# Optimization experiments

Measured on AMD Instinct MI355X. Metric: run time of the kernel, lower is better.

Reference implementation:

```python
import jax, jax.numpy as jnp
import numpy as np

EPS = 1e-5


def _two_qubit_block(xa, xb, pa, pb, ga, gb):
    """Analytic 2-qubit state-vector sim (real amplitudes, Ry/CNOT only).
    Circuit: Ry(xa)q0, Ry(xb)q1, Ry(pa)q0, Ry(pb)q1, CNOT(0,1), Ry(ga)q0, Ry(gb)q1.
    Returns (<Z0>, <Z1>) batched over xa/xb shape."""
    ha = 0.5 * (xa + pa)  # consecutive Ry angles add
    hb = 0.5 * (xb + pb)
    ca, sa = jnp.cos(ha), jnp.sin(ha)
    cb, sb = jnp.cos(hb), jnp.sin(hb)
    # product state amplitudes psi[i,j]
    p00, p01, p10, p11 = ca * cb, ca * sb, sa * cb, sa * sb
    # CNOT(control=0, target=1): swap |10> <-> |11>
    p10, p11 = p11, p10
    # Ry(ga) on qubit 0
    cg, sg = jnp.cos(0.5 * ga), jnp.sin(0.5 * ga)
    q00 = cg * p00 - sg * p10
    q10 = sg * p00 + cg * p10
    q01 = cg * p01 - sg * p11
    q11 = sg * p01 + cg * p11
    # Ry(gb) on qubit 1
    ch, sh = jnp.cos(0.5 * gb), jnp.sin(0.5 * gb)
    r00 = ch * q00 - sh * q01
    r01 = sh * q00 + ch * q01
    r10 = ch * q10 - sh * q11
    r11 = sh * q10 + ch * q11
    z0 = r00 ** 2 + r01 ** 2 - r10 ** 2 - r11 ** 2
    z1 = r00 ** 2 - r01 ** 2 + r10 ** 2 - r11 ** 2
    return z0, z1


def _forward(x, qparams, in_proj_w, in_proj_b, out_proj_w, out_proj_b,
             ln_w, ln_b, lin_w, lin_b):
    B = x.shape[0]
    xi = x.reshape(B, 28, 28)
    # extract 2x2 patches in order [x[r,c], x[r,c+1], x[r+1,c], x[r+1,c+1]]
    patches = xi.reshape(B, 14, 2, 14, 2).transpose(0, 1, 3, 2, 4).reshape(B, 196, 4)
    # vectorized quantum kernel: qubits (0,1) and (2,3) are independent 2-qubit blocks
    z0, z1 = _two_qubit_block(patches[..., 0], patches[..., 1],
                              qparams[0], qparams[1], qparams[4], qparams[5])
    z2, z3 = _two_qubit_block(patches[..., 2], patches[..., 3],
                              qparams[2], qparams[3], qparams[6], qparams[7])
    seq = jnp.stack([z0, z1, z2, z3], axis=-1)  # (B, 196, 4)

    # MultiheadAttention: embed_dim=4, heads=2, head_dim=2 (eval mode, no dropout)
    E, H, D, L = 4, 2, 2, 196
    qkv = seq @ in_proj_w.T + in_proj_b  # (B, L, 12)
    q, k, v = jnp.split(qkv, 3, axis=-1)
    q = q.reshape(B, L, H, D)
    k = k.reshape(B, L, H, D)
    v = v.reshape(B, L, H, D)
    scores = jnp.einsum('blhd,bmhd->bhlm', q, k) / jnp.sqrt(jnp.asarray(D, q.dtype))
    attn = jax.nn.softmax(scores, axis=-1)
    o = jnp.einsum('bhlm,bmhd->blhd', attn, v).reshape(B, L, E)
    o = o @ out_proj_w.T + out_proj_b  # (B, L, 4)

    # LayerNorm over the channel dim (size 4)
    mu = o.mean(axis=-1, keepdims=True)
    var = o.var(axis=-1, keepdims=True)
    o = (o - mu) / jnp.sqrt(var + EPS) * ln_w + ln_b

    # permute to (B, 4, 196) then flatten to match linear's 4*14*14 layout
    flat = o.transpose(0, 2, 1).reshape(B, 4 * 196)
    logits = flat @ lin_w.T + lin_b
    return jax.nn.log_softmax(logits, axis=-1)


def setup_inputs() -> dict:
    key = jax.random.key(0)
    ks = jax.random.split(key, 8)
    B, E, L = 2048, 4, 196
    x = jax.random.uniform(ks[0], (B, 1, 28, 28), dtype=jnp.float32)
    qparams = jax.random.normal(ks[1], (8,), dtype=jnp.float32)
    in_proj_w = jax.random.normal(ks[2], (3 * E, E), dtype=jnp.float32) * (1.0 / np.sqrt(E))
    in_proj_b = jnp.zeros((3 * E,), dtype=jnp.float32)
    out_proj_w = jax.random.normal(ks[3], (E, E), dtype=jnp.float32) * (1.0 / np.sqrt(E))
    out_proj_b = jnp.zeros((E,), dtype=jnp.float32)
    ln_w = jnp.ones((E,), dtype=jnp.float32)
    ln_b = jnp.zeros((E,), dtype=jnp.float32)
    lin_w = jax.random.normal(ks[4], (10, E * L), dtype=jnp.float32) * (1.0 / np.sqrt(E * L))
    lin_b = jnp.zeros((10,), dtype=jnp.float32)
    return {"x": x, "qparams": qparams, "in_proj_w": in_proj_w, "in_proj_b": in_proj_b,
            "out_proj_w": out_proj_w, "out_proj_b": out_proj_b,
            "ln_w": ln_w, "ln_b": ln_b, "lin_w": lin_w, "lin_b": lin_b}


def reference(x, qparams, in_proj_w, in_proj_b, out_proj_w, out_proj_b,
              ln_w, ln_b, lin_w, lin_b):
    return _forward(x, qparams, in_proj_w, in_proj_b, out_proj_w, out_proj_b,
                    ln_w, ln_b, lin_w, lin_b)
```

## Files before the change

### kernel.cpp

```cpp
#include <hip/hip_runtime.h>
#include <hip/hip_bf16.h>

#define NTHREADS 256
#define EPSF 1e-5f
#define QSCALE 1.0201606003163899f

typedef float v2f __attribute__((ext_vector_type(2)));
typedef float v4f __attribute__((ext_vector_type(4)));

#if __has_builtin(__builtin_amdgcn_exp2f)
#define EXP2F(x) __builtin_amdgcn_exp2f(x)
#else
extern "C" __device__ float __ocml_native_exp2_f32(float);
#define EXP2F(x) __ocml_native_exp2_f32(x)
#endif

__device__ __forceinline__ void two_qubit(float xa, float xb, float pa, float pb,
                                          float cg, float sg, float ch, float sh,
                                          float& z0, float& z1) {
    const float ha = 0.5f * (xa + pa);
    const float hb = 0.5f * (xb + pb);
    float sa, ca, sb, cb;
    __sincosf(ha, &sa, &ca);
    __sincosf(hb, &sb, &cb);
    const float p00 = ca * cb, p01 = ca * sb;
    const float p10 = sa * sb, p11 = sa * cb;
    const float q00 = cg * p00 - sg * p10;
    const float q10 = sg * p00 + cg * p10;
    const float q01 = cg * p01 - sg * p11;
    const float q11 = sg * p01 + cg * p11;
    const float r00 = ch * q00 - sh * q01;
    const float r01 = sh * q00 + ch * q01;
    const float r10 = ch * q10 - sh * q11;
    const float r11 = sh * q10 + ch * q11;
    const float a = r00 * r00, b = r01 * r01, c = r10 * r10, d = r11 * r11;
    z0 = a + b - c - d;
    z1 = a - b + c - d;
}

__global__ __launch_bounds__(NTHREADS, 8)
void quanv_fused(const float* __restrict__ x,
                 const float* __restrict__ qparams,
                 const float* __restrict__ in_w,
                 const float* __restrict__ in_b,
                 const float* __restrict__ out_w,
                 const float* __restrict__ out_b,
                 const float* __restrict__ lnw,
                 const float* __restrict__ lnb,
                 const float* __restrict__ lin_w,
                 const float* __restrict__ lin_b,
                 float* __restrict__ out)
{
    __shared__ __align__(16) float uni[2352];
    __shared__ __align__(16) float2 qs[2][196];
    __shared__ v4f kT[2][98];
    __shared__ v4f vT[2][98];
    __shared__ float w_in[48], b_in[12], w_out[16], b_out[4];
    __shared__ float s_lnw[4], s_lnb[4], s_linb[10];
    __shared__ float qc[8];
    __shared__ float qp[4];
    __shared__ float wsum[4][10];
    __shared__ float logits_s[10];
    __shared__ float lse_s;

    float* psum = uni;
    float* pa0  = uni + 784;
    float* pa1  = uni + 1568;
    float* flat = (float*)qs;

    const int tid = threadIdx.x;
    const int bid = blockIdx.x;

    const float4* xb4 = (const float4*)(x + (size_t)bid * 784);
    if (tid < 196) ((float4*)uni)[tid] = xb4[tid];
    if (tid < 48) w_in[tid] = in_w[tid];
    {
        int t = tid - 64;  if (t >= 0 && t < 12) b_in[t] = in_b[t];
        t = tid - 80;      if (t >= 0 && t < 16) w_out[t] = out_w[t];
        t = tid - 96;      if (t >= 0 && t < 4)  b_out[t] = out_b[t];
        t = tid - 112;     if (t >= 0 && t < 4)  s_lnw[t] = lnw[t];
        t = tid - 128;     if (t >= 0 && t < 4)  s_lnb[t] = lnb[t];
        t = tid - 144;     if (t >= 0 && t < 10) s_linb[t] = lin_b[t];
        t = tid - 160;     if (t >= 0 && t < 4)  qp[t] = qparams[t];
        t = tid - 176;
        if (t >= 0 && t < 4) {
            const float g = 0.5f * qparams[4 + t];
            float sg, cg;
            __sincosf(g, &sg, &cg);
            qc[2 * t] = cg;
            qc[2 * t + 1] = sg;
        }
    }
    __syncthreads();

    if (tid < 196) {
        const int l = tid;
        const int r = l / 14, c = l % 14;
        const float p0 = uni[(2 * r) * 28 + 2 * c];
        const float p1 = uni[(2 * r) * 28 + 2 * c + 1];
        const float p2 = uni[(2 * r + 1) * 28 + 2 * c];
        const float p3 = uni[(2 * r + 1) * 28 + 2 * c + 1];
        float z0, z1, z2, z3;
        two_qubit(p0, p1, qp[0], qp[1], qc[0], qc[1], qc[2], qc[3], z0, z1);
        two_qubit(p2, p3, qp[2], qp[3], qc[4], qc[5], qc[6], qc[7], z2, z3);
        float a[12];
        #pragma unroll
        for (int j = 0; j < 12; ++j)
            a[j] = b_in[j] + z0 * w_in[j * 4] + z1 * w_in[j * 4 + 1]
                 + z2 * w_in[j * 4 + 2] + z3 * w_in[j * 4 + 3];
        qs[0][l] = make_float2(a[0] * QSCALE, a[1] * QSCALE);
        qs[1][l] = make_float2(a[2] * QSCALE, a[3] * QSCALE);
        const int i4 = l >> 1, e = l & 1;
        ((float*)&kT[0][i4])[e]     = a[4];
        ((float*)&kT[0][i4])[2 + e] = a[5];
        ((float*)&kT[1][i4])[e]     = a[6];
        ((float*)&kT[1][i4])[2 + e] = a[7];
        ((float*)&vT[0][i4])[e]     = a[8];
        ((float*)&vT[0][i4])[2 + e] = a[9];
        ((float*)&vT[1][i4])[e]     = a[10];
        ((float*)&vT[1][i4])[2 + e] = a[11];
    }
    __syncthreads();

    const int wv = tid >> 6;
    const int lane = tid & 63;
    const int h = wv >> 1;
    const int hs = wv & 1;
    const int i0 = hs * 49;
    const int pbase = h * 392 + hs * 196;
    {
        float qx[3], qy[3];
        v2f sum2[3], ac0[3], ac1[3];
        #pragma unroll
        for (int r = 0; r < 3; ++r) {
            const float2 q = qs[h][lane + r * 64];
            qx[r] = q.x;
            qy[r] = q.y;
            sum2[r] = (v2f){0.f, 0.f};
            ac0[r]  = (v2f){0.f, 0.f};
            ac1[r]  = (v2f){0.f, 0.f};
        }
        const v4f* kTp = &kT[h][i0];
        const v4f* vTp = &vT[h][i0];

        auto body = [&](v4f kk, v4f vv) {
            const v2f kxy = kk.xy, kzw = kk.zw;
            const v2f vxy = vv.xy, vzw = vv.zw;
            #pragma unroll
            for (int r = 0; r < 3; ++r) {
                const v2f s = kxy * qx[r] + kzw * qy[r];
                v2f e;
                e.x = EXP2F(s.x);
                e.y = EXP2F(s.y);
                sum2[r] += e;
                ac0[r]  += e * vxy;
                ac1[r]  += e * vzw;
            }
        };

        v4f kk = kTp[0];
        v4f vv = vTp[0];
        #pragma unroll 6
        for (int i = 0; i < 48; ++i) {
            const v4f kkn = kTp[i + 1];
            const v4f vvn = vTp[i + 1];
            body(kk, vv);
            kk = kkn;
            vv = vvn;
        }
        body(kk, vv);

        #pragma unroll
        for (int r = 0; r < 3; ++r) {
            const int l = lane + r * 64;
            psum[pbase + l] = sum2[r].x + sum2[r].y;
            pa0[pbase + l]  = ac0[r].x + ac0[r].y;
            pa1[pbase + l]  = ac1[r].x + ac1[r].y;
        }
    }
    {
        const int g = lane >> 4, s16 = lane & 15;
        const int l = 192 + g;
        const float2 q = qs[h][l];
        const v4f* kTp = &kT[h][0];
        const v4f* vTp = &vT[h][0];
        v2f sum2 = {0.f, 0.f}, ac0 = {0.f, 0.f}, ac1 = {0.f, 0.f};
        #pragma unroll
        for (int k = 0; k < 3; ++k) {
            const int i = i0 + s16 + k * 16;
            const v4f kk = kTp[i];
            const v4f vv = vTp[i];
            const v2f s = kk.xy * q.x + kk.zw * q.y;
            v2f e;
            e.x = EXP2F(s.x);
            e.y = EXP2F(s.y);
            sum2 += e;
            ac0 += e * vv.xy;
            ac1 += e * vv.zw;
        }
        if (s16 == 0) {
            const v4f kk = kTp[i0 + 48];
            const v4f vv = vTp[i0 + 48];
            const v2f s = kk.xy * q.x + kk.zw * q.y;
            v2f e;
            e.x = EXP2F(s.x);
            e.y = EXP2F(s.y);
            sum2 += e;
            ac0 += e * vv.xy;
            ac1 += e * vv.zw;
        }
        float sum = sum2.x + sum2.y;
        float a0  = ac0.x + ac0.y;
        float a1  = ac1.x + ac1.y;
        #pragma unroll
        for (int off = 1; off < 16; off <<= 1) {
            sum += __shfl_xor(sum, off);
            a0  += __shfl_xor(a0, off);
            a1  += __shfl_xor(a1, off);
        }
        if (s16 == 0) {
            psum[pbase + l] = sum;
            pa0[pbase + l]  = a0;
            pa1[pbase + l]  = a1;
        }
    }
    __syncthreads();

    if (tid < 196) {
        const int l = tid;
        const float s0 = psum[l]       + psum[196 + l];
        const float s1 = psum[392 + l] + psum[588 + l];
        const float i0h = 1.0f / s0, i1h = 1.0f / s1;
        const float f0 = (pa0[l]       + pa0[196 + l]) * i0h;
        const float f1 = (pa1[l]       + pa1[196 + l]) * i0h;
        const float f2 = (pa0[392 + l] + pa0[588 + l]) * i1h;
        const float f3 = (pa1[392 + l] + pa1[588 + l]) * i1h;
        const float e0 = b_out[0] + f0 * w_out[0]  + f1 * w_out[1]  + f2 * w_out[2]  + f3 * w_out[3];
        const float e1 = b_out[1] + f0 * w_out[4]  + f1 * w_out[5]  + f2 * w_out[6]  + f3 * w_out[7];
        const float e2 = b_out[2] + f0 * w_out[8]  + f1 * w_out[9]  + f2 * w_out[10] + f3 * w_out[11];
        const float e3 = b_out[3] + f0 * w_out[12] + f1 * w_out[13] + f2 * w_out[14] + f3 * w_out[15];
        const float mu = 0.25f * (e0 + e1 + e2 + e3);
        const float d0 = e0 - mu, d1 = e1 - mu, d2 = e2 - mu, d3 = e3 - mu;
        const float var = 0.25f * (d0 * d0 + d1 * d1 + d2 * d2 + d3 * d3);
        const float rs = rsqrtf(var + EPSF);
        flat[0 * 196 + l] = d0 * rs * s_lnw[0] + s_lnb[0];
        flat[1 * 196 + l] = d1 * rs * s_lnw[1] + s_lnb[1];
        flat[2 * 196 + l] = d2 * rs * s_lnw[2] + s_lnb[2];
        flat[3 * 196 + l] = d3 * rs * s_lnw[3] + s_lnb[3];
    }
    __syncthreads();

    float part[10];
    #pragma unroll
    for (int j = 0; j < 10; ++j) part[j] = 0.f;
    if (tid < 196) {
        const float4 f = ((const float4*)flat)[tid];
        const float4* lw = (const float4*)lin_w + tid;
        #pragma unroll
        for (int j = 0; j < 10; ++j) {
            const float4 w = lw[j * 196];
            part[j] = f.x * w.x + f.y * w.y + f.z * w.z + f.w * w.w;
        }
    }
    #pragma unroll
    for (int j = 0; j < 10; ++j) {
        float v = part[j];
        #pragma unroll
        for (int off = 32; off > 0; off >>= 1) v += __shfl_down(v, off);
        if (lane == 0) wsum[wv][j] = v;
    }
    __syncthreads();
    if (tid < 10)
        logits_s[tid] = wsum[0][tid] + wsum[1][tid] + wsum[2][tid]
                      + wsum[3][tid] + s_linb[tid];
    __syncthreads();
    if (tid == 0) {
        float mx = logits_s[0];
        #pragma unroll
        for (int j = 1; j < 10; ++j) mx = fmaxf(mx, logits_s[j]);
        float se = 0.f;
        #pragma unroll
        for (int j = 0; j < 10; ++j) se += __expf(logits_s[j] - mx);
        lse_s = mx + __logf(se);
    }
    __syncthreads();
    if (tid < 10) out[(size_t)bid * 10 + tid] = logits_s[tid] - lse_s;
}

extern "C" void kernel_launch(void* const* d_in, const int* in_sizes, int n_in,
                              void* d_out, int out_size, void* d_ws, size_t ws_size,
                              hipStream_t stream) {
    const float* x        = (const float*)d_in[0];
    const float* qparams  = (const float*)d_in[1];
    const float* in_w     = (const float*)d_in[2];
    const float* in_b     = (const float*)d_in[3];
    const float* out_w    = (const float*)d_in[4];
    const float* out_b    = (const float*)d_in[5];
    const float* lnw      = (const float*)d_in[6];
    const float* lnb      = (const float*)d_in[7];
    const float* lin_w    = (const float*)d_in[8];
    const float* lin_b    = (const float*)d_in[9];
    float* out            = (float*)d_out;

    const int B = in_sizes[0] / 784;
    hipLaunchKernelGGL(quanv_fused, dim3(B), dim3(NTHREADS), 0, stream,
                       x, qparams, in_w, in_b, out_w, out_b, lnw, lnb, lin_w, lin_b, out);
}
```

Measured before the change: 38.35 us.

## Process two images per 512-thread block and simplify attention loop

Each block now handles two batch images with 512 threads, halving the block count and sharing the parameter loads across two images. Shared-memory buffers are doubled and indexed per image, and the partial-score scratch reuses the image buffer per image. The hand-pipelined key/value prefetch loop is replaced by a plain loop unrolled by 7. The risks are higher LDS use per block, which may reduce occupancy, and dropping the min-blocks hint from launch bounds.

New measurement: 38.53 us. About the same (+0.5%).

```diff
diff --git a/kernel.cpp b/kernel.cpp
--- a/kernel.cpp
+++ b/kernel.cpp
@@ -1,7 +1,7 @@
 #include <hip/hip_runtime.h>
 #include <hip/hip_bf16.h>
 
-#define NTHREADS 256
+#define NTHREADS 512
 #define EPSF 1e-5f
 #define QSCALE 1.0201606003163899f
 
@@ -38,7 +38,7 @@
     z1 = a - b + c - d;
 }
 
-__global__ __launch_bounds__(NTHREADS, 8)
+__global__ __launch_bounds__(NTHREADS)
 void quanv_fused(const float* __restrict__ x,
                  const float* __restrict__ qparams,
                  const float* __restrict__ in_w,
@@ -49,30 +49,30 @@
                  const float* __restrict__ lnb,
                  const float* __restrict__ lin_w,
                  const float* __restrict__ lin_b,
-                 float* __restrict__ out)
+                 float* __restrict__ out,
+                 int B)
 {
-    __shared__ __align__(16) float uni[2352];
-    __shared__ __align__(16) float2 qs[2][196];
-    __shared__ v4f kT[2][98];
-    __shared__ v4f vT[2][98];
+    __shared__ __align__(16) float uni[2][2352];
+    __shared__ __align__(16) float2 qs[2][2][196];
+    __shared__ v4f kT[2][2][98];
+    __shared__ v4f vT[2][2][98];
     __shared__ float w_in[48], b_in[12], w_out[16], b_out[4];
     __shared__ float s_lnw[4], s_lnb[4], s_linb[10];
     __shared__ float qc[8];
     __shared__ float qp[4];
-    __shared__ float wsum[4][10];
-    __shared__ float logits_s[10];
-    __shared__ float lse_s;
-
-    float* psum = uni;
-    float* pa0  = uni + 784;
-    float* pa1  = uni + 1568;
-    float* flat = (float*)qs;
+    __shared__ float wsum[8][10];
+    __shared__ float logits_s[2][10];
+    __shared__ float lse_s[2];
 
     const int tid = threadIdx.x;
     const int bid = blockIdx.x;
-
-    const float4* xb4 = (const float4*)(x + (size_t)bid * 784);
-    if (tid < 196) ((float4*)uni)[tid] = xb4[tid];
+    const int timg = tid >> 8;
+    const int tl   = tid & 255;
+    const int gimg = 2 * bid + timg;
+    const int gsrc = (gimg < B) ? gimg : (B - 1);
+
+    const float4* xb4 = (const float4*)(x + (size_t)gsrc * 784);
+    if (tl < 196) ((float4*)uni[timg])[tl] = xb4[tl];
     if (tid < 48) w_in[tid] = in_w[tid];
     {
         int t = tid - 64;  if (t >= 0 && t < 12) b_in[t] = in_b[t];
@@ -93,13 +93,14 @@
     }
     __syncthreads();
 
-    if (tid < 196) {
-        const int l = tid;
+    if (tl < 196) {
+        const int l = tl;
+        const float* img = uni[timg];
         const int r = l / 14, c = l % 14;
-        const float p0 = uni[(2 * r) * 28 + 2 * c];
-        const float p1 = uni[(2 * r) * 28 + 2 * c + 1];
-        const float p2 = uni[(2 * r + 1) * 28 + 2 * c];
-        const float p3 = uni[(2 * r + 1) * 28 + 2 * c + 1];
+        const float p0 = img[(2 * r) * 28 + 2 * c];
+        const float p1 = img[(2 * r) * 28 + 2 * c + 1];
+        const float p2 = img[(2 * r + 1) * 28 + 2 * c];
+        const float p3 = img[(2 * r + 1) * 28 + 2 * c + 1];
         float z0, z1, z2, z3;
         two_qubit(p0, p1, qp[0], qp[1], qc[0], qc[1], qc[2], qc[3], z0, z1);
         two_qubit(p2, p3, qp[2], qp[3], qc[4], qc[5], qc[6], qc[7], z2, z3);
@@ -108,42 +109,48 @@
         for (int j = 0; j < 12; ++j)
             a[j] = b_in[j] + z0 * w_in[j * 4] + z1 * w_in[j * 4 + 1]
                  + z2 * w_in[j * 4 + 2] + z3 * w_in[j * 4 + 3];
-        qs[0][l] = make_float2(a[0] * QSCALE, a[1] * QSCALE);
-        qs[1][l] = make_float2(a[2] * QSCALE, a[3] * QSCALE);
+        qs[timg][0][l] = make_float2(a[0] * QSCALE, a[1] * QSCALE);
+        qs[timg][1][l] = make_float2(a[2] * QSCALE, a[3] * QSCALE);
         const int i4 = l >> 1, e = l & 1;
-        ((float*)&kT[0][i4])[e]     = a[4];
-        ((float*)&kT[0][i4])[2 + e] = a[5];
-        ((float*)&kT[1][i4])[e]     = a[6];
-        ((float*)&kT[1][i4])[2 + e] = a[7];
-        ((float*)&vT[0][i4])[e]     = a[8];
-        ((float*)&vT[0][i4])[2 + e] = a[9];
-        ((float*)&vT[1][i4])[e]     = a[10];
-        ((float*)&vT[1][i4])[2 + e] = a[11];
-    }
-    __syncthreads();
-
-    const int wv = tid >> 6;
+        ((float*)&kT[timg][0][i4])[e]     = a[4];
+        ((float*)&kT[timg][0][i4])[2 + e] = a[5];
+        ((float*)&kT[timg][1][i4])[e]     = a[6];
+        ((float*)&kT[timg][1][i4])[2 + e] = a[7];
+        ((float*)&vT[timg][0][i4])[e]     = a[8];
+        ((float*)&vT[timg][0][i4])[2 + e] = a[9];
+        ((float*)&vT[timg][1][i4])[e]     = a[10];
+        ((float*)&vT[timg][1][i4])[2 + e] = a[11];
+    }
+    __syncthreads();
+
+    const int wv   = tid >> 6;
     const int lane = tid & 63;
-    const int h = wv >> 1;
-    const int hs = wv & 1;
-    const int i0 = hs * 49;
+    const int aimg = wv >> 2;
+    const int h    = (wv >> 1) & 1;
+    const int hs   = wv & 1;
+    const int i0   = hs * 49;
+    float* psum = uni[aimg];
+    float* pa0  = uni[aimg] + 784;
+    float* pa1  = uni[aimg] + 1568;
     const int pbase = h * 392 + hs * 196;
     {
         float qx[3], qy[3];
         v2f sum2[3], ac0[3], ac1[3];
         #pragma unroll
         for (int r = 0; r < 3; ++r) {
-            const float2 q = qs[h][lane + r * 64];
+            const float2 q = qs[aimg][h][lane + r * 64];
             qx[r] = q.x;
             qy[r] = q.y;
             sum2[r] = (v2f){0.f, 0.f};
             ac0[r]  = (v2f){0.f, 0.f};
             ac1[r]  = (v2f){0.f, 0.f};
         }
-        const v4f* kTp = &kT[h][i0];
-        const v4f* vTp = &vT[h][i0];
-
-        auto body = [&](v4f kk, v4f vv) {
+        const v4f* kTp = &kT[aimg][h][i0];
+        const v4f* vTp = &vT[aimg][h][i0];
+        #pragma unroll 7
+        for (int i = 0; i < 49; ++i) {
+            const v4f kk = kTp[i];
+            const v4f vv = vTp[i];
             const v2f kxy = kk.xy, kzw = kk.zw;
             const v2f vxy = vv.xy, vzw = vv.zw;
             #pragma unroll
@@ -156,20 +163,7 @@
                 ac0[r]  += e * vxy;
                 ac1[r]  += e * vzw;
             }
-        };
-
-        v4f kk = kTp[0];
-        v4f vv = vTp[0];
-        #pragma unroll 6
-        for (int i = 0; i < 48; ++i) {
-            const v4f kkn = kTp[i + 1];
-            const v4f vvn = vTp[i + 1];
-            body(kk, vv);
-            kk = kkn;
-            vv = vvn;
-        }
-        body(kk, vv);
-
+        }
         #pragma unroll
         for (int r = 0; r < 3; ++r) {
             const int l = lane + r * 64;
@@ -181,9 +175,9 @@
     {
         const int g = lane >> 4, s16 = lane & 15;
         const int l = 192 + g;
-        const float2 q = qs[h][l];
-        const v4f* kTp = &kT[h][0];
-        const v4f* vTp = &vT[h][0];
+        const float2 q = qs[aimg][h][l];
+        const v4f* kTp = &kT[aimg][h][0];
+        const v4f* vTp = &vT[aimg][h][0];
         v2f sum2 = {0.f, 0.f}, ac0 = {0.f, 0.f}, ac1 = {0.f, 0.f};
         #pragma unroll
         for (int k = 0; k < 3; ++k) {
@@ -226,15 +220,19 @@
     }
     __syncthreads();
 
-    if (tid < 196) {
-        const int l = tid;
-        const float s0 = psum[l]       + psum[196 + l];
-        const float s1 = psum[392 + l] + psum[588 + l];
+    float* flat = (float*)qs[timg];
+    if (tl < 196) {
+        const int l = tl;
+        const float* ps = uni[timg];
+        const float* p0 = uni[timg] + 784;
+        const float* p1 = uni[timg] + 1568;
+        const float s0 = ps[l]       + ps[196 + l];
+        const float s1 = ps[392 + l] + ps[588 + l];
         const float i0h = 1.0f / s0, i1h = 1.0f / s1;
-        const float f0 = (pa0[l]       + pa0[196 + l]) * i0h;
-        const float f1 = (pa1[l]       + pa1[196 + l]) * i0h;
-        const float f2 = (pa0[392 + l] + pa0[588 + l]) * i1h;
-        const float f3 = (pa1[392 + l] + pa1[588 + l]) * i1h;
+        const float f0 = (p0[l]       + p0[196 + l]) * i0h;
+        const float f1 = (p1[l]       + p1[196 + l]) * i0h;
+        const float f2 = (p0[392 + l] + p0[588 + l]) * i1h;
+        const float f3 = (p1[392 + l] + p1[588 + l]) * i1h;
         const float e0 = b_out[0] + f0 * w_out[0]  + f1 * w_out[1]  + f2 * w_out[2]  + f3 * w_out[3];
         const float e1 = b_out[1] + f0 * w_out[4]  + f1 * w_out[5]  + f2 * w_out[6]  + f3 * w_out[7];
         const float e2 = b_out[2] + f0 * w_out[8]  + f1 * w_out[9]  + f2 * w_out[10] + f3 * w_out[11];
@@ -253,9 +251,9 @@
     float part[10];
     #pragma unroll
     for (int j = 0; j < 10; ++j) part[j] = 0.f;
-    if (tid < 196) {
-        const float4 f = ((const float4*)flat)[tid];
-        const float4* lw = (const float4*)lin_w + tid;
+    if (tl < 196) {
+        const float4 f = ((const float4*)flat)[tl];
+        const float4* lw = (const float4*)lin_w + tl;
         #pragma unroll
         for (int j = 0; j < 10; ++j) {
             const float4 w = lw[j * 196];
@@ -270,21 +268,23 @@
         if (lane == 0) wsum[wv][j] = v;
     }
     __syncthreads();
-    if (tid < 10)
-        logits_s[tid] = wsum[0][tid] + wsum[1][tid] + wsum[2][tid]
-                      + wsum[3][tid] + s_linb[tid];
-    __syncthreads();
-    if (tid == 0) {
-        float mx = logits_s[0];
-        #pragma unroll
-        for (int j = 1; j < 10; ++j) mx = fmaxf(mx, logits_s[j]);
+    if (tl < 10)
+        logits_s[timg][tl] = wsum[timg * 4 + 0][tl] + wsum[timg * 4 + 1][tl]
+                           + wsum[timg * 4 + 2][tl] + wsum[timg * 4 + 3][tl]
+                           + s_linb[tl];
+    __syncthreads();
+    if (tl == 0) {
+        float mx = logits_s[timg][0];
+        #pragma unroll
+        for (int j = 1; j < 10; ++j) mx = fmaxf(mx, logits_s[timg][j]);
         float se = 0.f;
         #pragma unroll
-        for (int j = 0; j < 10; ++j) se += __expf(logits_s[j] - mx);
-        lse_s = mx + __logf(se);
-    }
-    __syncthreads();
-    if (tid < 10) out[(size_t)bid * 10 + tid] = logits_s[tid] - lse_s;
+        for (int j = 0; j < 10; ++j) se += __expf(logits_s[timg][j] - mx);
+        lse_s[timg] = mx + __logf(se);
+    }
+    __syncthreads();
+    if (tl < 10 && gimg < B)
+        out[(size_t)gimg * 10 + tl] = logits_s[timg][tl] - lse_s[timg];
 }
 
 extern "C" void kernel_launch(void* const* d_in, const int* in_sizes, int n_in,
@@ -303,6 +303,7 @@
     float* out            = (float*)d_out;
 
     const int B = in_sizes[0] / 784;
-    hipLaunchKernelGGL(quanv_fused, dim3(B), dim3(NTHREADS), 0, stream,
-                       x, qparams, in_w, in_b, out_w, out_b, lnw, lnb, lin_w, lin_b, out);
+    const int nblk = (B + 1) / 2;
+    hipLaunchKernelGGL(quanv_fused, dim3(nblk), dim3(NTHREADS), 0, stream,
+                       x, qparams, in_w, in_b, out_w, out_b, lnw, lnb, lin_w, lin_b, out, B);
 }
```

## Split fused kernel into per-head attention kernel and separate tail kernel

Applied to the files above, without the earlier changes.

Replaces the single 256-thread block per image with two kernels. The first launches one 64-thread block per image and head, recomputes the quantum features and that head's Q/K/V, runs the full attention, and writes normalized head outputs to a workspace buffer. The second kernel reads that buffer and does the out-projection, layernorm, final linear and log-softmax with one wave per image. This removes block-wide barriers and the cross-wave partial-sum merge, but the quantum feature computation is done twice per image and the intermediate now makes a round trip through global memory with an extra launch.

After: 43.03 us. +12.2%, slower.

```diff
diff --git a/kernel.cpp b/kernel.cpp
--- a/kernel.cpp
+++ b/kernel.cpp
@@ -1,7 +1,6 @@
 #include <hip/hip_runtime.h>
 #include <hip/hip_bf16.h>
 
-#define NTHREADS 256
 #define EPSF 1e-5f
 #define QSCALE 1.0201606003163899f
 
@@ -38,112 +37,82 @@
     z1 = a - b + c - d;
 }
 
-__global__ __launch_bounds__(NTHREADS, 8)
-void quanv_fused(const float* __restrict__ x,
-                 const float* __restrict__ qparams,
-                 const float* __restrict__ in_w,
-                 const float* __restrict__ in_b,
-                 const float* __restrict__ out_w,
-                 const float* __restrict__ out_b,
-                 const float* __restrict__ lnw,
-                 const float* __restrict__ lnb,
-                 const float* __restrict__ lin_w,
-                 const float* __restrict__ lin_b,
-                 float* __restrict__ out)
+__global__ __launch_bounds__(64)
+void quanv_attn(const float* __restrict__ x,
+                const float* __restrict__ qparams,
+                const float* __restrict__ in_w,
+                const float* __restrict__ in_b,
+                float2* __restrict__ ws)
 {
-    __shared__ __align__(16) float uni[2352];
-    __shared__ __align__(16) float2 qs[2][196];
-    __shared__ v4f kT[2][98];
-    __shared__ v4f vT[2][98];
-    __shared__ float w_in[48], b_in[12], w_out[16], b_out[4];
-    __shared__ float s_lnw[4], s_lnb[4], s_linb[10];
-    __shared__ float qc[8];
-    __shared__ float qp[4];
-    __shared__ float wsum[4][10];
-    __shared__ float logits_s[10];
-    __shared__ float lse_s;
-
-    float* psum = uni;
-    float* pa0  = uni + 784;
-    float* pa1  = uni + 1568;
-    float* flat = (float*)qs;
-
-    const int tid = threadIdx.x;
-    const int bid = blockIdx.x;
-
-    const float4* xb4 = (const float4*)(x + (size_t)bid * 784);
-    if (tid < 196) ((float4*)uni)[tid] = xb4[tid];
-    if (tid < 48) w_in[tid] = in_w[tid];
+    __shared__ __align__(16) float img[784];
+    __shared__ v4f kT[98];
+    __shared__ v4f vT[98];
+    __shared__ float w6[24], b6[6], qp_s[4], qc_s[8];
+
+    const int lane = threadIdx.x;
+    const int bid  = blockIdx.x;
+    const int im   = bid >> 1;
+    const int h    = bid & 1;
+
+    const float4* xb4 = (const float4*)(x + (size_t)im * 784);
+    #pragma unroll
+    for (int r = 0; r < 3; ++r) ((float4*)img)[lane + 64 * r] = xb4[lane + 64 * r];
+    if (lane < 4) ((float4*)img)[192 + lane] = xb4[192 + lane];
+    if (lane < 24) {
+        const int j6 = lane >> 2;
+        w6[lane] = in_w[((j6 >> 1) * 4 + 2 * h + (j6 & 1)) * 4 + (lane & 3)];
+    }
+    { int t = lane - 24; if (t >= 0 && t < 6)  b6[t] = in_b[(t >> 1) * 4 + 2 * h + (t & 1)]; }
+    { int t = lane - 32; if (t >= 0 && t < 4)  qp_s[t] = qparams[t]; }
+    { int t = lane - 40;
+      if (t >= 0 && t < 4) {
+          const float g = 0.5f * qparams[4 + t];
+          float sg, cg;
+          __sincosf(g, &sg, &cg);
+          qc_s[2 * t] = cg; qc_s[2 * t + 1] = sg;
+      } }
+    __syncthreads();
+
+    float qx[4], qy[4];
+    #pragma unroll
+    for (int r = 0; r < 4; ++r) {
+        const int l = (r < 3) ? (lane + 64 * r) : (192 + lane);
+        if (r == 3 && lane >= 4) break;
+        const int rr = l / 14, cc = l % 14;
+        const float p0 = img[(2 * rr) * 28 + 2 * cc];
+        const float p1 = img[(2 * rr) * 28 + 2 * cc + 1];
+        const float p2 = img[(2 * rr + 1) * 28 + 2 * cc];
+        const float p3 = img[(2 * rr + 1) * 28 + 2 * cc + 1];
+        float z0, z1, z2, z3;
+        two_qubit(p0, p1, qp_s[0], qp_s[1], qc_s[0], qc_s[1], qc_s[2], qc_s[3], z0, z1);
+        two_qubit(p2, p3, qp_s[2], qp_s[3], qc_s[4], qc_s[5], qc_s[6], qc_s[7], z2, z3);
+        float a[6];
+        #pragma unroll
+        for (int j = 0; j < 6; ++j)
+            a[j] = b6[j] + z0 * w6[j * 4] + z1 * w6[j * 4 + 1]
+                 + z2 * w6[j * 4 + 2] + z3 * w6[j * 4 + 3];
+        qx[r] = a[0] * QSCALE;
+        qy[r] = a[1] * QSCALE;
+        const int i4 = l >> 1, e = l & 1;
+        ((float*)&kT[i4])[e]     = a[2];
+        ((float*)&kT[i4])[2 + e] = a[3];
+        ((float*)&vT[i4])[e]     = a[4];
+        ((float*)&vT[i4])[2 + e] = a[5];
+    }
+    __syncthreads();
+
     {
-        int t = tid - 64;  if (t >= 0 && t < 12) b_in[t] = in_b[t];
-        t = tid - 80;      if (t >= 0 && t < 16) w_out[t] = out_w[t];
-        t = tid - 96;      if (t >= 0 && t < 4)  b_out[t] = out_b[t];
-        t = tid - 112;     if (t >= 0 && t < 4)  s_lnw[t] = lnw[t];
-        t = tid - 128;     if (t >= 0 && t < 4)  s_lnb[t] = lnb[t];
-        t = tid - 144;     if (t >= 0 && t < 10) s_linb[t] = lin_b[t];
-        t = tid - 160;     if (t >= 0 && t < 4)  qp[t] = qparams[t];
-        t = tid - 176;
-        if (t >= 0 && t < 4) {
-            const float g = 0.5f * qparams[4 + t];
-            float sg, cg;
-            __sincosf(g, &sg, &cg);
-            qc[2 * t] = cg;
-            qc[2 * t + 1] = sg;
-        }
-    }
-    __syncthreads();
-
-    if (tid < 196) {
-        const int l = tid;
-        const int r = l / 14, c = l % 14;
-        const float p0 = uni[(2 * r) * 28 + 2 * c];
-        const float p1 = uni[(2 * r) * 28 + 2 * c + 1];
-        const float p2 = uni[(2 * r + 1) * 28 + 2 * c];
-        const float p3 = uni[(2 * r + 1) * 28 + 2 * c + 1];
-        float z0, z1, z2, z3;
-        two_qubit(p0, p1, qp[0], qp[1], qc[0], qc[1], qc[2], qc[3], z0, z1);
-        two_qubit(p2, p3, qp[2], qp[3], qc[4], qc[5], qc[6], qc[7], z2, z3);
-        float a[12];
-        #pragma unroll
-        for (int j = 0; j < 12; ++j)
-            a[j] = b_in[j] + z0 * w_in[j * 4] + z1 * w_in[j * 4 + 1]
-                 + z2 * w_in[j * 4 + 2] + z3 * w_in[j * 4 + 3];
-        qs[0][l] = make_float2(a[0] * QSCALE, a[1] * QSCALE);
-        qs[1][l] = make_float2(a[2] * QSCALE, a[3] * QSCALE);
-        const int i4 = l >> 1, e = l & 1;
-        ((float*)&kT[0][i4])[e]     = a[4];
-        ((float*)&kT[0][i4])[2 + e] = a[5];
-        ((float*)&kT[1][i4])[e]     = a[6];
-        ((float*)&kT[1][i4])[2 + e] = a[7];
-        ((float*)&vT[0][i4])[e]     = a[8];
-        ((float*)&vT[0][i4])[2 + e] = a[9];
-        ((float*)&vT[1][i4])[e]     = a[10];
-        ((float*)&vT[1][i4])[2 + e] = a[11];
-    }
-    __syncthreads();
-
-    const int wv = tid >> 6;
-    const int lane = tid & 63;
-    const int h = wv >> 1;
-    const int hs = wv & 1;
-    const int i0 = hs * 49;
-    const int pbase = h * 392 + hs * 196;
-    {
-        float qx[3], qy[3];
         v2f sum2[3], ac0[3], ac1[3];
         #pragma unroll
         for (int r = 0; r < 3; ++r) {
-            const float2 q = qs[h][lane + r * 64];
-            qx[r] = q.x;
-            qy[r] = q.y;
             sum2[r] = (v2f){0.f, 0.f};
             ac0[r]  = (v2f){0.f, 0.f};
             ac1[r]  = (v2f){0.f, 0.f};
         }
-        const v4f* kTp = &kT[h][i0];
-        const v4f* vTp = &vT[h][i0];
-
-        auto body = [&](v4f kk, v4f vv) {
+        #pragma unroll 7
+        for (int i = 0; i < 98; ++i) {
+            const v4f kk = kT[i];
+            const v4f vv = vT[i];
             const v2f kxy = kk.xy, kzw = kk.zw;
             const v2f vxy = vv.xy, vzw = vv.zw;
             #pragma unroll
@@ -156,62 +125,51 @@
                 ac0[r]  += e * vxy;
                 ac1[r]  += e * vzw;
             }
-        };
-
-        v4f kk = kTp[0];
-        v4f vv = vTp[0];
-        #pragma unroll 6
-        for (int i = 0; i < 48; ++i) {
-            const v4f kkn = kTp[i + 1];
-            const v4f vvn = vTp[i + 1];
-            body(kk, vv);
-            kk = kkn;
-            vv = vvn;
-        }
-        body(kk, vv);
-
+        }
         #pragma unroll
         for (int r = 0; r < 3; ++r) {
-            const int l = lane + r * 64;
-            psum[pbase + l] = sum2[r].x + sum2[r].y;
-            pa0[pbase + l]  = ac0[r].x + ac0[r].y;
-            pa1[pbase + l]  = ac1[r].x + ac1[r].y;
+            const int l = lane + 64 * r;
+            const float sum = sum2[r].x + sum2[r].y;
+            const float inv = 1.0f / sum;
+            const float a0 = (ac0[r].x + ac0[r].y) * inv;
+            const float a1 = (ac1[r].x + ac1[r].y) * inv;
+            ws[(size_t)im * 392 + l * 2 + h] = make_float2(a0, a1);
         }
     }
     {
-        const int g = lane >> 4, s16 = lane & 15;
-        const int l = 192 + g;
-        const float2 q = qs[h][l];
-        const v4f* kTp = &kT[h][0];
-        const v4f* vTp = &vT[h][0];
-        v2f sum2 = {0.f, 0.f}, ac0 = {0.f, 0.f}, ac1 = {0.f, 0.f};
-        #pragma unroll
-        for (int k = 0; k < 3; ++k) {
-            const int i = i0 + s16 + k * 16;
-            const v4f kk = kTp[i];
-            const v4f vv = vTp[i];
-            const v2f s = kk.xy * q.x + kk.zw * q.y;
+        const int grp = lane >> 4, s16 = lane & 15;
+        const int l = 192 + grp;
+        const float tqx = __shfl(qx[3], grp);
+        const float tqy = __shfl(qy[3], grp);
+        v2f S = {0.f, 0.f}, A0 = {0.f, 0.f}, A1 = {0.f, 0.f};
+        #pragma unroll
+        for (int k = 0; k < 6; ++k) {
+            const int i = s16 + 16 * k;
+            const v4f kk = kT[i];
+            const v4f vv = vT[i];
+            const v2f s = kk.xy * tqx + kk.zw * tqy;
             v2f e;
             e.x = EXP2F(s.x);
             e.y = EXP2F(s.y);
-            sum2 += e;
-            ac0 += e * vv.xy;
-            ac1 += e * vv.zw;
-        }
-        if (s16 == 0) {
-            const v4f kk = kTp[i0 + 48];
-            const v4f vv = vTp[i0 + 48];
-            const v2f s = kk.xy * q.x + kk.zw * q.y;
+            S  += e;
+            A0 += e * vv.xy;
+            A1 += e * vv.zw;
+        }
+        if (s16 < 2) {
+            const int i = 96 + s16;
+            const v4f kk = kT[i];
+            const v4f vv = vT[i];
+            const v2f s = kk.xy * tqx + kk.zw * tqy;
             v2f e;
             e.x = EXP2F(s.x);
             e.y = EXP2F(s.y);
-            sum2 += e;
-            ac0 += e * vv.xy;
-            ac1 += e * vv.zw;
-        }
-        float sum = sum2.x + sum2.y;
-        float a0  = ac0.x + ac0.y;
-        float a1  = ac1.x + ac1.y;
+            S  += e;
+            A0 += e * vv.xy;
+            A1 += e * vv.zw;
+        }
+        float sum = S.x + S.y;
+        float a0  = A0.x + A0.y;
+        float a1  = A1.x + A1.y;
         #pragma unroll
         for (int off = 1; off < 16; off <<= 1) {
             sum += __shfl_xor(sum, off);
@@ -219,72 +177,94 @@
             a1  += __shfl_xor(a1, off);
         }
         if (s16 == 0) {
-            psum[pbase + l] = sum;
-            pa0[pbase + l]  = a0;
-            pa1[pbase + l]  = a1;
-        }
-    }
-    __syncthreads();
-
-    if (tid < 196) {
-        const int l = tid;
-        const float s0 = psum[l]       + psum[196 + l];
-        const float s1 = psum[392 + l] + psum[588 + l];
-        const float i0h = 1.0f / s0, i1h = 1.0f / s1;
-        const float f0 = (pa0[l]       + pa0[196 + l]) * i0h;
-        const float f1 = (pa1[l]       + pa1[196 + l]) * i0h;
-        const float f2 = (pa0[392 + l] + pa0[588 + l]) * i1h;
-        const float f3 = (pa1[392 + l] + pa1[588 + l]) * i1h;
-        const float e0 = b_out[0] + f0 * w_out[0]  + f1 * w_out[1]  + f2 * w_out[2]  + f3 * w_out[3];
-        const float e1 = b_out[1] + f0 * w_out[4]  + f1 * w_out[5]  + f2 * w_out[6]  + f3 * w_out[7];
-        const float e2 = b_out[2] + f0 * w_out[8]  + f1 * w_out[9]  + f2 * w_out[10] + f3 * w_out[11];
-        const float e3 = b_out[3] + f0 * w_out[12] + f1 * w_out[13] + f2 * w_out[14] + f3 * w_out[15];
-        const float mu = 0.25f * (e0 + e1 + e2 + e3);
-        const float d0 = e0 - mu, d1 = e1 - mu, d2 = e2 - mu, d3 = e3 - mu;
-        const float var = 0.25f * (d0 * d0 + d1 * d1 + d2 * d2 + d3 * d3);
-        const float rs = rsqrtf(var + EPSF);
-        flat[0 * 196 + l] = d0 * rs * s_lnw[0] + s_lnb[0];
-        flat[1 * 196 + l] = d1 * rs * s_lnw[1] + s_lnb[1];
-        flat[2 * 196 + l] = d2 * rs * s_lnw[2] + s_lnb[2];
-        flat[3 * 196 + l] = d3 * rs * s_lnw[3] + s_lnb[3];
+            const float inv = 1.0f / sum;
+            ws[(size_t)im * 392 + l * 2 + h] = make_float2(a0 * inv, a1 * inv);
+        }
+    }
+}
+
+__global__ __launch_bounds__(64)
+void quanv_tail(const float2* __restrict__ ws,
+                const float* __restrict__ out_w,
+                const float* __restrict__ out_b,
+                const float* __restrict__ lnw,
+                const float* __restrict__ lnb,
+                const float* __restrict__ lin_w,
+                const float* __restrict__ lin_b,
+                float* __restrict__ out)
+{
+    __shared__ __align__(16) float flat[784];
+    __shared__ float w_out[16], b_out[4], s_lnw[4], s_lnb[4], s_linb[10];
+
+    const int lane = threadIdx.x;
+    const int im   = blockIdx.x;
+
+    if (lane < 16) w_out[lane] = out_w[lane];
+    { int t = lane - 16; if (t >= 0 && t < 4)  b_out[t] = out_b[t]; }
+    { int t = lane - 24; if (t >= 0 && t < 4)  s_lnw[t] = lnw[t]; }
+    { int t = lane - 32; if (t >= 0 && t < 4)  s_lnb[t] = lnb[t]; }
+    { int t = lane - 40; if (t >= 0 && t < 10) s_linb[t] = lin_b[t]; }
+    __syncthreads();
+
+    const float4* ob4 = (const float4*)(ws + (size_t)im * 392);
+    #pragma unroll
+    for (int r = 0; r < 4; ++r) {
+        const int l = lane + 64 * r;
+        if (l < 196) {
+            const float4 f = ob4[l];
+            const float f0 = f.x, f1 = f.y, f2 = f.z, f3 = f.w;
+            const float e0 = b_out[0] + f0 * w_out[0]  + f1 * w_out[1]  + f2 * w_out[2]  + f3 * w_out[3];
+            const float e1 = b_out[1] + f0 * w_out[4]  + f1 * w_out[5]  + f2 * w_out[6]  + f3 * w_out[7];
+            const float e2 = b_out[2] + f0 * w_out[8]  + f1 * w_out[9]  + f2 * w_out[10] + f3 * w_out[11];
+            const float e3 = b_out[3] + f0 * w_out[12] + f1 * w_out[13] + f2 * w_out[14] + f3 * w_out[15];
+            const float mu = 0.25f * (e0 + e1 + e2 + e3);
+            const float d0 = e0 - mu, d1 = e1 - mu, d2 = e2 - mu, d3 = e3 - mu;
+            const float var = 0.25f * (d0 * d0 + d1 * d1 + d2 * d2 + d3 * d3);
+            const float rs = rsqrtf(var + EPSF);
+            flat[0 * 196 + l] = d0 * rs * s_lnw[0] + s_lnb[0];
+            flat[1 * 196 + l] = d1 * rs * s_lnw[1] + s_lnb[1];
+            flat[2 * 196 + l] = d2 * rs * s_lnw[2] + s_lnb[2];
+            flat[3 * 196 + l] = d3 * rs * s_lnw[3] + s_lnb[3];
+        }
     }
     __syncthreads();
 
     float part[10];
     #pragma unroll
     for (int j = 0; j < 10; ++j) part[j] = 0.f;
-    if (tid < 196) {
-        const float4 f = ((const float4*)flat)[tid];
-        const float4* lw = (const float4*)lin_w + tid;
+    #pragma unroll
+    for (int r = 0; r < 4; ++r) {
+        const int i = lane + 64 * r;
+        if (i < 196) {
+            const float4 f = ((const float4*)flat)[i];
+            const float4* lw = (const float4*)lin_w + i;
+            #pragma unroll
+            for (int j = 0; j < 10; ++j) {
+                const float4 w = lw[j * 196];
+                part[j] += f.x * w.x + f.y * w.y + f.z * w.z + f.w * w.w;
+            }
+        }
+    }
+    #pragma unroll
+    for (int j = 0; j < 10; ++j) {
+        #pragma unroll
+        for (int off = 32; off > 0; off >>= 1) part[j] += __shfl_down(part[j], off);
+    }
+    if (lane == 0) {
+        float lg[10];
+        float mx = -1e30f;
         #pragma unroll
         for (int j = 0; j < 10; ++j) {
-            const float4 w = lw[j * 196];
-            part[j] = f.x * w.x + f.y * w.y + f.z * w.z + f.w * w.w;
-        }
-    }
-    #pragma unroll
-    for (int j = 0; j < 10; ++j) {
-        float v = part[j];
-        #pragma unroll
-        for (int off = 32; off > 0; off >>= 1) v += __shfl_down(v, off);
-        if (lane == 0) wsum[wv][j] = v;
-    }
-    __syncthreads();
-    if (tid < 10)
-        logits_s[tid] = wsum[0][tid] + wsum[1][tid] + wsum[2][tid]
-                      + wsum[3][tid] + s_linb[tid];
-    __syncthreads();
-    if (tid == 0) {
-        float mx = logits_s[0];
-        #pragma unroll
-        for (int j = 1; j < 10; ++j) mx = fmaxf(mx, logits_s[j]);
+            lg[j] = part[j] + s_linb[j];
+            mx = fmaxf(mx, lg[j]);
+        }
         float se = 0.f;
         #pragma unroll
-        for (int j = 0; j < 10; ++j) se += __expf(logits_s[j] - mx);
-        lse_s = mx + __logf(se);
-    }
-    __syncthreads();
-    if (tid < 10) out[(size_t)bid * 10 + tid] = logits_s[tid] - lse_s;
+        for (int j = 0; j < 10; ++j) se += __expf(lg[j] - mx);
+        const float lse = mx + __logf(se);
+        #pragma unroll
+        for (int j = 0; j < 10; ++j) out[(size_t)im * 10 + j] = lg[j] - lse;
+    }
 }
 
 extern "C" void kernel_launch(void* const* d_in, const int* in_sizes, int n_in,
@@ -301,8 +281,11 @@
     const float* lin_w    = (const float*)d_in[8];
     const float* lin_b    = (const float*)d_in[9];
     float* out            = (float*)d_out;
-
-    const int B = in_sizes[0] / 784;
-    hipLaunchKernelGGL(quanv_fused, dim3(B), dim3(NTHREADS), 0, stream,
-                       x, qparams, in_w, in_b, out_w, out_b, lnw, lnb, lin_w, lin_b, out);
-}
+    float2* ws            = (float2*)d_ws;
+
+    const int nimg = in_sizes[0] / 784;
+    hipLaunchKernelGGL(quanv_attn, dim3(nimg * 2), dim3(64), 0, stream,
+                       x, qparams, in_w, in_b, ws);
+    hipLaunchKernelGGL(quanv_tail, dim3(nimg), dim3(64), 0, stream,
+                       ws, out_w, out_b, lnw, lnb, lin_w, lin_b, out);
+}
```
